# Kernel optimization log

Hardware: AMD Instinct MI355X
Metric: run time of the kernel (lower is better)

The kernel has to match this reference:

```python
import jax, jax.numpy as jnp
import numpy as np

N = 50000      # nodes
E = 800000     # edges (before self-loops)
DIN = 2        # dim_input
DEMB = 128     # dim_embedding
H = 8          # n_heads
DV = 16        # dim_values (H*DV == DEMB)
DH = 512       # dim_hidden
L = 2          # n_att_layers
K = 10         # APPNP steps
ALPHA = 0.1
EPS = 1e-5     # BatchNorm eps
NEG_SLOPE = 0.2  # GAT leaky_relu slope


def setup_inputs() -> dict:
    key = jax.random.key(0)
    ks = jax.random.split(key, 16)
    s = 0.05
    inp = {}
    inp["x"] = jax.random.normal(ks[0], (N, DIN), jnp.float32)
    inp["J"] = jax.random.uniform(ks[1], (N, 1), jnp.float32)
    inp["edge_index"] = jax.random.randint(ks[2], (2, E), 0, N, jnp.int32)
    # Lin1: Linear(dim_input+1, dim_embedding)
    inp["lin0_w"] = jax.random.normal(ks[3], (DIN + 1, DEMB), jnp.float32) * s
    inp["lin0_b"] = jnp.zeros((DEMB,), jnp.float32)
    # Per attention layer (stacked over L):
    inp["gat_w"]   = jax.random.normal(ks[4], (L, DEMB, H * DV), jnp.float32) * s
    inp["att_src"] = jax.random.normal(ks[5], (L, H, DV), jnp.float32) * s
    inp["att_dst"] = jax.random.normal(ks[6], (L, H, DV), jnp.float32) * s
    inp["lin1_w"]  = jax.random.normal(ks[7], (L, DV, DEMB), jnp.float32) * s
    inp["bn1_g"]   = jnp.ones((L, DEMB), jnp.float32)
    inp["bn1_b"]   = jnp.zeros((L, DEMB), jnp.float32)
    inp["lin2_w"]  = jax.random.normal(ks[8], (L, DEMB, DH), jnp.float32) * s
    inp["lin2_b"]  = jnp.zeros((L, DH), jnp.float32)
    inp["lin3_w"]  = jax.random.normal(ks[9], (L, DH, DEMB), jnp.float32) * s
    inp["lin3_b"]  = jnp.zeros((L, DEMB), jnp.float32)
    inp["bn2_g"]   = jnp.ones((L, DEMB), jnp.float32)
    inp["bn2_b"]   = jnp.zeros((L, DEMB), jnp.float32)
    return inp


def _bn(z, g, b):
    # BatchNorm1d over nodes, training-mode batch statistics (biased var)
    mu = z.mean(0)
    var = jnp.mean((z - mu) ** 2, axis=0)
    return g * (z - mu) * jax.lax.rsqrt(var + EPS) + b


def reference(x, J, edge_index, lin0_w, lin0_b, gat_w, att_src, att_dst,
              lin1_w, bn1_g, bn1_b, lin2_w, lin2_b, lin3_w, lin3_b,
              bn2_g, bn2_b):
    # add self-loops (PyG GATConv and APPNP defaults)
    loop = jnp.arange(N, dtype=edge_index.dtype)
    src = jnp.concatenate([edge_index[0], loop])  # message source j
    dst = jnp.concatenate([edge_index[1], loop])  # message target i

    h = jnp.concatenate([x, J], axis=1) @ lin0_w + lin0_b  # [N, DEMB]

    for l in range(L):
        # ---- GATConv ----
        xl = (h @ gat_w[l]).reshape(N, H, DV)                # [N,H,DV]
        a_s = (xl * att_src[l]).sum(-1)                      # [N,H]
        a_d = (xl * att_dst[l]).sum(-1)                      # [N,H]
        e = jax.nn.leaky_relu(a_s[src] + a_d[dst], NEG_SLOPE)  # [E',H]
        e = e - jax.ops.segment_max(e, dst, num_segments=N)[dst]
        ee = jnp.exp(e)
        alpha = ee / jax.ops.segment_sum(ee, dst, num_segments=N)[dst]
        msg = xl[src] * alpha[:, :, None]                    # [E',H,DV]
        gat_out = jax.ops.segment_sum(msg, dst, num_segments=N)  # [N,H,DV]
        # lin1 per head then sum over heads
        hsum = jnp.einsum('nhc,cd->nd', gat_out, lin1_w[l])  # [N,DEMB]
        h1 = _bn(h + hsum, bn1_g[l], bn1_b[l])
        h2 = jax.nn.relu(h1 @ lin2_w[l] + lin2_b[l]) @ lin3_w[l] + lin3_b[l]
        h = _bn(h2 + h1, bn2_g[l], bn2_b[l])

    # ---- APPNP: K steps of (1-a)*Ahat h + a*h0, Ahat = D^-1/2 (A+I) D^-1/2 ----
    deg = jax.ops.segment_sum(jnp.ones_like(dst, jnp.float32), dst, num_segments=N)
    dinv = jax.lax.rsqrt(jnp.maximum(deg, 1.0))  # self-loops guarantee deg>=1
    norm = (dinv[src] * dinv[dst])[:, None]      # [E',1]
    h0 = h

    def step(hk, _):
        agg = jax.ops.segment_sum(norm * hk[src], dst, num_segments=N)
        return (1.0 - ALPHA) * agg + ALPHA * h0, None

    h, _ = jax.lax.scan(step, h, None, length=K)
    return jnp.concatenate([h, J], axis=1)  # [N, DEMB+1]
```

## Files before the change

### kernel.cpp

```cpp
#include <hip/hip_runtime.h>

#define NN 50000
#define NE 800000
#define EP (NE + NN)
#define DEMB 128
#define DHID 512
#define CHUNK 12800
#define NB_SCAN 196

typedef unsigned short ushort_t;
typedef __attribute__((ext_vector_type(8))) short short8_t;
typedef __attribute__((ext_vector_type(4))) float float4_t;

__device__ __forceinline__ float bf2f(ushort_t u) {
    return __uint_as_float(((unsigned int)u) << 16);
}
__device__ __forceinline__ ushort_t f2bf(float f) {
    unsigned int x = __float_as_uint(f);
    x += 0x7fffu + ((x >> 16) & 1u);
    return (ushort_t)(x >> 16);
}
__device__ __forceinline__ float lo16(unsigned int w) { return __uint_as_float(w << 16); }
__device__ __forceinline__ float hi16(unsigned int w) { return __uint_as_float(w & 0xffff0000u); }
__device__ __forceinline__ unsigned int pack2(float a, float b) {
    return (unsigned int)f2bf(a) | ((unsigned int)f2bf(b) << 16);
}
static inline int cdiv(int a, int b) { return (a + b - 1) / b; }

__global__ void k_detect(const unsigned int* __restrict__ Jw, int* __restrict__ flag) {
    if (threadIdx.x != 0 || blockIdx.x != 0) return;
    int votes = 0;
    for (int i = 0; i < 8; ++i) {
        unsigned int w = Jw[i];
        unsigned int ex = (w >> 23) & 0xFFu;
        if ((w >> 31) == 0u && ex >= 100u && ex <= 126u) votes++;
    }
    *flag = (votes >= 6) ? 1 : 0;
}

struct CvtArgs {
    const void* src[16];
    float* dst[16];
    int n[16];
};
__global__ void k_cvt_all(CvtArgs a, const int* __restrict__ flag) {
    int which = blockIdx.y;
    int i = blockIdx.x * 256 + threadIdx.x;
    if (i >= a.n[which]) return;
    float v;
    if (*flag) v = ((const float*)a.src[which])[i];
    else       v = bf2f(((const ushort_t*)a.src[which])[i]);
    a.dst[which][i] = v;
}

struct TrArgs {
    const float* src[6];
    ushort_t* dst[6];
    int K[6];
    int Nc[6];
};
__global__ void k_tr_all(TrArgs a) {
    int which = blockIdx.y;
    int idx = blockIdx.x * 256 + threadIdx.x;
    int K = a.K[which], Nc = a.Nc[which];
    if (idx >= K * Nc) return;
    int k = idx / Nc, n = idx - k * Nc;
    a.dst[which][n * K + k] = f2bf(a.src[which][idx]);
}

__global__ void k_deg(const int* __restrict__ ei, int* __restrict__ deg) {
    int e = blockIdx.x * 256 + threadIdx.x;
    if (e >= EP) return;
    int d = (e < NE) ? ei[NE + e] : (e - NE);
    atomicAdd(&deg[d], 1);
}

__global__ void k_part(const int* __restrict__ deg, int* __restrict__ part) {
    __shared__ int sm[256];
    int i = blockIdx.x * 256 + threadIdx.x;
    int v = (i < NN) ? deg[i] : 0;
    sm[threadIdx.x] = v;
    __syncthreads();
    for (int off = 128; off > 0; off >>= 1) {
        if (threadIdx.x < off) sm[threadIdx.x] += sm[threadIdx.x + off];
        __syncthreads();
    }
    if (threadIdx.x == 0) part[blockIdx.x] = sm[0];
}

__global__ void k_scan2(const int* __restrict__ part, int* __restrict__ poff,
                        int* __restrict__ rowp) {
    __shared__ int sm[256];
    int t = threadIdx.x;
    int v = (t < NB_SCAN) ? part[t] : 0;
    sm[t] = v;
    __syncthreads();
    int incl = v;
    for (int off = 1; off < 256; off <<= 1) {
        int u = (t >= off) ? sm[t - off] : 0;
        __syncthreads();
        incl += u;
        sm[t] = incl;
        __syncthreads();
    }
    if (t < NB_SCAN) poff[t] = incl - v;
    if (t == 255) rowp[NN] = sm[255];
}

__global__ void k_rowp(const int* __restrict__ deg, const int* __restrict__ poff,
                       int* __restrict__ rowp, float* __restrict__ dinv) {
    __shared__ int sm[256];
    int i = blockIdx.x * 256 + threadIdx.x;
    int t = threadIdx.x;
    int v = (i < NN) ? deg[i] : 0;
    sm[t] = v;
    __syncthreads();
    int incl = v;
    for (int off = 1; off < 256; off <<= 1) {
        int u = (t >= off) ? sm[t - off] : 0;
        __syncthreads();
        incl += u;
        sm[t] = incl;
        __syncthreads();
    }
    if (i < NN) {
        rowp[i] = poff[blockIdx.x] + incl - v;
        dinv[i] = rsqrtf(fmaxf((float)v, 1.0f));
    }
}

__global__ void k_fill(const int* __restrict__ ei, int* __restrict__ fillpos,
                       ushort_t* __restrict__ col) {
    int e = blockIdx.x * 256 + threadIdx.x;
    if (e >= EP) return;
    int s, d;
    if (e < NE) { s = ei[e]; d = ei[NE + e]; } else { s = d = e - NE; }
    int pos = atomicAdd(&fillpos[d], 1);
    col[pos] = (ushort_t)s;
}

__global__ void k_lin0(const float* __restrict__ x, const float* __restrict__ J,
                       const float* __restrict__ w, const float* __restrict__ b,
                       float* __restrict__ h, ushort_t* __restrict__ hB) {
    int idx = blockIdx.x * 256 + threadIdx.x;
    if (idx >= NN * DEMB) return;
    int n = idx >> 7, d = idx & 127;
    float v = x[n * 2] * w[d] + x[n * 2 + 1] * w[DEMB + d] + J[n] * w[2 * DEMB + d] + b[d];
    h[idx] = v;
    hB[idx] = f2bf(v);
}

__global__ void k_att(const unsigned int* __restrict__ xlB, const float* __restrict__ asrc,
                      const float* __restrict__ adst, float* __restrict__ a_s,
                      float* __restrict__ a_d) {
    int idx = blockIdx.x * 256 + threadIdx.x;
    if (idx >= NN * 8) return;
    int n = idx >> 3, hh = idx & 7;
    const unsigned int* row = xlB + (size_t)n * 64 + hh * 8;
    float s = 0.f, d = 0.f;
#pragma unroll
    for (int c = 0; c < 8; ++c) {
        unsigned int w = row[c];
        float v0 = lo16(w), v1 = hi16(w);
        s += v0 * asrc[hh * 16 + 2 * c] + v1 * asrc[hh * 16 + 2 * c + 1];
        d += v0 * adst[hh * 16 + 2 * c] + v1 * adst[hh * 16 + 2 * c + 1];
    }
    a_s[idx] = s;
    a_d[idx] = d;
}

__global__ __launch_bounds__(256) void k_z1s(const float* __restrict__ h, const float* __restrict__ g,
                                             const float* __restrict__ w1,
                                             float* __restrict__ stats) {
    int d = threadIdx.x & 127;
    int rstart = blockIdx.x * 2 + (threadIdx.x >> 7);
    int stride = gridDim.x * 2;
    float s1 = 0.f, s2 = 0.f;
    for (int r = rstart; r < NN; r += stride) {
        const float* gr = g + r * 16;
        float s = h[(size_t)r * DEMB + d];
#pragma unroll
        for (int c = 0; c < 16; ++c) s += gr[c] * w1[c * DEMB + d];
        s1 += s;
        s2 += s * s;
    }
    __shared__ float b1[256], b2[256];
    b1[threadIdx.x] = s1;
    b2[threadIdx.x] = s2;
    __syncthreads();
    if (threadIdx.x < 128) {
        atomicAdd(&stats[threadIdx.x], b1[threadIdx.x] + b1[threadIdx.x + 128]);
        atomicAdd(&stats[128 + threadIdx.x], b2[threadIdx.x] + b2[threadIdx.x + 128]);
    }
}

__global__ void k_bnapply1(const float* __restrict__ h, const float* __restrict__ g,
                           const float* __restrict__ w1, const float* __restrict__ stats,
                           const float* __restrict__ gam, const float* __restrict__ bet,
                           float* __restrict__ outF, ushort_t* __restrict__ outB) {
    int idx = blockIdx.x * 256 + threadIdx.x;
    if (idx >= NN * DEMB) return;
    int n = idx >> 7, d = idx & 127;
    float s = h[idx];
    const float* gr = g + n * 16;
#pragma unroll
    for (int c = 0; c < 16; ++c) s += gr[c] * w1[c * DEMB + d];
    const float invN = 1.0f / (float)NN;
    float mu = stats[d] * invN;
    float var = stats[128 + d] * invN - mu * mu;
    float rs = rsqrtf(fmaxf(var, 0.f) + 1e-5f);
    float v = gam[d] * (s - mu) * rs + bet[d];
    outF[idx] = v;
    outB[idx] = f2bf(v);
}

__global__ void k_bnapply(const float* __restrict__ z, const float* __restrict__ stats,
                          const float* __restrict__ gam, const float* __restrict__ bet,
                          float* __restrict__ outF, ushort_t* __restrict__ outB) {
    int idx = blockIdx.x * 256 + threadIdx.x;
    if (idx >= NN * DEMB) return;
    int d = idx & 127;
    const float invN = 1.0f / (float)NN;
    float mu = stats[d] * invN;
    float var = stats[128 + d] * invN - mu * mu;
    float rs = rsqrtf(fmaxf(var, 0.f) + 1e-5f);
    float v = gam[d] * (z[idx] - mu) * rs + bet[d];
    outF[idx] = v;
    outB[idx] = f2bf(v);
}

__global__ void k_bnapply_fin(const float* __restrict__ z, const float* __restrict__ stats,
                              const float* __restrict__ gam, const float* __restrict__ bet,
                              const float* __restrict__ dinv,
                              unsigned int* __restrict__ hs, unsigned int* __restrict__ h0p) {
    int idx = blockIdx.x * 256 + threadIdx.x;
    if (idx >= NN * 64) return;
    int n = idx >> 6, d0 = (idx & 63) * 2;
    const float invN = 1.0f / (float)NN;
    float2 zv = ((const float2*)z)[idx];
    float mu0 = stats[d0] * invN, mu1 = stats[d0 + 1] * invN;
    float v0 = stats[128 + d0] * invN - mu0 * mu0;
    float v1 = stats[128 + d0 + 1] * invN - mu1 * mu1;
    float rs0 = rsqrtf(fmaxf(v0, 0.f) + 1e-5f);
    float rs1 = rsqrtf(fmaxf(v1, 0.f) + 1e-5f);
    float a = gam[d0] * (zv.x - mu0) * rs0 + bet[d0];
    float b = gam[d0 + 1] * (zv.y - mu1) * rs1 + bet[d0 + 1];
    float di = dinv[n];
    hs[idx] = pack2(di * a, di * b);
    h0p[idx] = pack2(a, b);
}

__global__ __launch_bounds__(256) void k_gat(const int* __restrict__ rowp,
                                             const ushort_t* __restrict__ col,
                                             const float* __restrict__ a_s, const float* __restrict__ a_d,
                                             const unsigned int* __restrict__ xlB, float* __restrict__ g) {
    int wid = (blockIdx.x * 256 + threadIdx.x) >> 6;
    int lane = threadIdx.x & 63;
    if (wid >= NN) return;
    int p0 = rowp[wid], p1 = rowp[wid + 1];
    int hh = lane >> 3;
    float ad2 = a_d[wid * 8 + hh];
    float acc0 = 0.f, acc1 = 0.f, s = 0.f;
    int p = p0;
    while (p < p1) {
        int cnt = p1 - p;
        if (cnt > 64) cnt = 64;
        int pl = p + lane;
        int jv = (int)col[pl < p1 ? pl : (p1 - 1)];
        int i = 0;
        for (; i + 8 <= cnt; i += 8) {
            int j0 = __shfl(jv, i),     j1 = __shfl(jv, i + 1);
            int j2 = __shfl(jv, i + 2), j3 = __shfl(jv, i + 3);
            int j4 = __shfl(jv, i + 4), j5 = __shfl(jv, i + 5);
            int j6 = __shfl(jv, i + 6), j7 = __shfl(jv, i + 7);
            float e0 = a_s[j0 * 8 + hh] + ad2, e1 = a_s[j1 * 8 + hh] + ad2;
            float e2 = a_s[j2 * 8 + hh] + ad2, e3 = a_s[j3 * 8 + hh] + ad2;
            float e4 = a_s[j4 * 8 + hh] + ad2, e5 = a_s[j5 * 8 + hh] + ad2;
            float e6 = a_s[j6 * 8 + hh] + ad2, e7 = a_s[j7 * 8 + hh] + ad2;
            unsigned int w0 = xlB[j0 * 64 + lane], w1 = xlB[j1 * 64 + lane];
            unsigned int w2 = xlB[j2 * 64 + lane], w3 = xlB[j3 * 64 + lane];
            unsigned int w4 = xlB[j4 * 64 + lane], w5 = xlB[j5 * 64 + lane];
            unsigned int w6 = xlB[j6 * 64 + lane], w7 = xlB[j7 * 64 + lane];
            e0 = e0 > 0.f ? e0 : 0.2f * e0;  e1 = e1 > 0.f ? e1 : 0.2f * e1;
            e2 = e2 > 0.f ? e2 : 0.2f * e2;  e3 = e3 > 0.f ? e3 : 0.2f * e3;
            e4 = e4 > 0.f ? e4 : 0.2f * e4;  e5 = e5 > 0.f ? e5 : 0.2f * e5;
            e6 = e6 > 0.f ? e6 : 0.2f * e6;  e7 = e7 > 0.f ? e7 : 0.2f * e7;
            float al0 = __expf(e0), al1 = __expf(e1), al2 = __expf(e2), al3 = __expf(e3);
            float al4 = __expf(e4), al5 = __expf(e5), al6 = __expf(e6), al7 = __expf(e7);
            s += al0 + al1 + al2 + al3 + al4 + al5 + al6 + al7;
            acc0 += al0 * lo16(w0) + al1 * lo16(w1) + al2 * lo16(w2) + al3 * lo16(w3) +
                    al4 * lo16(w4) + al5 * lo16(w5) + al6 * lo16(w6) + al7 * lo16(w7);
            acc1 += al0 * hi16(w0) + al1 * hi16(w1) + al2 * hi16(w2) + al3 * hi16(w3) +
                    al4 * hi16(w4) + al5 * hi16(w5) + al6 * hi16(w6) + al7 * hi16(w7);
        }
        for (; i < cnt; ++i) {
            int j = __shfl(jv, i);
            float e = a_s[j * 8 + hh] + ad2;
            e = e > 0.f ? e : 0.2f * e;
            float al = __expf(e);
            unsigned int w = xlB[j * 64 + lane];
            s += al;
            acc0 += al * lo16(w);
            acc1 += al * hi16(w);
        }
        p += cnt;
    }
    float inv = 1.f / s;
    acc0 *= inv;
    acc1 *= inv;
    acc0 += __shfl_xor(acc0, 8);  acc1 += __shfl_xor(acc1, 8);
    acc0 += __shfl_xor(acc0, 16); acc1 += __shfl_xor(acc1, 16);
    acc0 += __shfl_xor(acc0, 32); acc1 += __shfl_xor(acc1, 32);
    if (lane < 8) ((float2*)g)[wid * 8 + lane] = make_float2(acc0, acc1);
}

__global__ __launch_bounds__(256) void k_appnp(const int* __restrict__ rowp,
                                               const ushort_t* __restrict__ col,
                                               const float* __restrict__ dinv,
                                               const unsigned int* __restrict__ hs,
                                               const unsigned int* __restrict__ h0p,
                                               unsigned int* __restrict__ hs_out,
                                               const float* __restrict__ Jf,
                                               const int* __restrict__ flag,
                                               void* __restrict__ out, int writeOut) {
    int wid = (blockIdx.x * 256 + threadIdx.x) >> 6;
    int lane = threadIdx.x & 63;
    if (wid >= NN) return;
    int p0 = rowp[wid], p1 = rowp[wid + 1];
    float a0 = 0.f, a1 = 0.f;
    int p = p0;
    while (p < p1) {
        int cnt = p1 - p;
        if (cnt > 64) cnt = 64;
        int pl = p + lane;
        int jv = (int)col[pl < p1 ? pl : (p1 - 1)];
        int i = 0;
        for (; i + 8 <= cnt; i += 8) {
            int j0 = __shfl(jv, i),     j1 = __shfl(jv, i + 1);
            int j2 = __shfl(jv, i + 2), j3 = __shfl(jv, i + 3);
            int j4 = __shfl(jv, i + 4), j5 = __shfl(jv, i + 5);
            int j6 = __shfl(jv, i + 6), j7 = __shfl(jv, i + 7);
            unsigned int w0 = hs[j0 * 64 + lane], w1 = hs[j1 * 64 + lane];
            unsigned int w2 = hs[j2 * 64 + lane], w3 = hs[j3 * 64 + lane];
            unsigned int w4 = hs[j4 * 64 + lane], w5 = hs[j5 * 64 + lane];
            unsigned int w6 = hs[j6 * 64 + lane], w7 = hs[j7 * 64 + lane];
            a0 += lo16(w0) + lo16(w1) + lo16(w2) + lo16(w3) +
                  lo16(w4) + lo16(w5) + lo16(w6) + lo16(w7);
            a1 += hi16(w0) + hi16(w1) + hi16(w2) + hi16(w3) +
                  hi16(w4) + hi16(w5) + hi16(w6) + hi16(w7);
        }
        for (; i < cnt; ++i) {
            int j = __shfl(jv, i);
            unsigned int w = hs[j * 64 + lane];
            a0 += lo16(w);
            a1 += hi16(w);
        }
        p += cnt;
    }
    float di = dinv[wid];
    unsigned int hw = h0p[(size_t)wid * 64 + lane];
    float n0 = 0.9f * di * a0 + 0.1f * lo16(hw);
    float n1 = 0.9f * di * a1 + 0.1f * hi16(hw);
    if (!writeOut) {
        hs_out[(size_t)wid * 64 + lane] = pack2(di * n0, di * n1);
    } else {
        size_t base = (size_t)wid * 129;
        if (*flag) {
            float* o = (float*)out;
            o[base + 2 * lane] = n0;
            o[base + 2 * lane + 1] = n1;
            if (lane == 0) o[base + 128] = Jf[wid];
        } else {
            ushort_t* o = (ushort_t*)out;
            o[base + 2 * lane] = f2bf(n0);
            o[base + 2 * lane + 1] = f2bf(n1);
            if (lane == 0) o[base + 128] = f2bf(Jf[wid]);
        }
    }
}

template <int MODE>
__global__ __launch_bounds__(256) void k_gemm_bt(const ushort_t* __restrict__ A,
                                                 const ushort_t* __restrict__ Bt,
                                                 int M, int K, int Nc,
                                                 const float* __restrict__ bias,
                                                 const float* __restrict__ res,
                                                 float* __restrict__ outF,
                                                 ushort_t* __restrict__ outB,
                                                 float* __restrict__ stats) {
    __shared__ __align__(16) ushort_t lsA[64 * 32];
    __shared__ __align__(16) ushort_t lsB[64 * 32];
    int t = threadIdx.x;
    int m0 = blockIdx.x * 64;
    int n0 = blockIdx.y * 64;
    int w = t >> 6, lane = t & 63;
    int row16 = lane & 15, quad = lane >> 4;
    float4_t acc[4];
#pragma unroll
    for (int nt = 0; nt < 4; ++nt) acc[nt] = (float4_t){0.f, 0.f, 0.f, 0.f};
    int srow = t >> 2;
    int scol = (t & 3) * 8;
    const int nK = K >> 5;
    for (int kb = 0; kb < nK; ++kb) {
        int k0 = kb << 5;
        uint4 va = make_uint4(0u, 0u, 0u, 0u);
        int ar = m0 + srow;
        if (ar < M) va = *(const uint4*)(A + (size_t)ar * K + k0 + scol);
        *(uint4*)(lsA + srow * 32 + scol) = va;
        uint4 vb = *(const uint4*)(Bt + (size_t)(n0 + srow) * K + k0 + scol);
        *(uint4*)(lsB + srow * 32 + scol) = vb;
        __syncthreads();
        short8_t af = *(const short8_t*)(lsA + (w * 16 + row16) * 32 + quad * 8);
#pragma unroll
        for (int nt = 0; nt < 4; ++nt) {
            short8_t bfv = *(const short8_t*)(lsB + (nt * 16 + row16) * 32 + quad * 8);
            acc[nt] = __builtin_amdgcn_mfma_f32_16x16x32_bf16(af, bfv, acc[nt], 0, 0, 0);
        }
        __syncthreads();
    }
    if (MODE == 2) {
        __shared__ float s1[64], s2[64];
        if (t < 64) { s1[t] = 0.f; s2[t] = 0.f; }
        __syncthreads();
#pragma unroll
        for (int nt = 0; nt < 4; ++nt) {
            int cb = nt * 16 + row16;
            int cc = n0 + cb;
            float bv = bias[cc];
            float ls = 0.f, lq = 0.f;
#pragma unroll
            for (int r = 0; r < 4; ++r) {
                int rr = m0 + w * 16 + quad * 4 + r;
                if (rr < M) {
                    float v = acc[nt][r] + bv + res[(size_t)rr * Nc + cc];
                    outF[(size_t)rr * Nc + cc] = v;
                    ls += v;
                    lq += v * v;
                }
            }
            atomicAdd(&s1[cb], ls);
            atomicAdd(&s2[cb], lq);
        }
        __syncthreads();
        if (t < 64) {
            atomicAdd(&stats[n0 + t], s1[t]);
            atomicAdd(&stats[128 + n0 + t], s2[t]);
        }
    } else {
#pragma unroll
        for (int nt = 0; nt < 4; ++nt) {
            int cc = n0 + nt * 16 + row16;
            float bv = (MODE == 1) ? bias[cc] : 0.f;
#pragma unroll
            for (int r = 0; r < 4; ++r) {
                int rr = m0 + w * 16 + quad * 4 + r;
                if (rr < M) {
                    float v = acc[nt][r];
                    if (MODE == 1) {
                        v += bv;
                        v = v > 0.f ? v : 0.f;
                        outB[(size_t)rr * Nc + cc] = f2bf(v);
                    } else {
                        outB[(size_t)rr * Nc + cc] = f2bf(v);
                    }
                }
            }
        }
    }
}

extern "C" void kernel_launch(void* const* d_in, const int* in_sizes, int n_in,
                              void* d_out, int out_size, void* d_ws, size_t ws_size,
                              hipStream_t stream) {
    const int* ei = (const int*)d_in[2];

    char* p = (char*)d_ws;
    auto alloc = [&](size_t bytes) {
        void* r = (void*)p;
        p += (bytes + 255) & ~(size_t)255;
        return r;
    };
    float*    Af    = (float*)alloc((size_t)NN * DEMB * 4);
    float*    Cf    = (float*)alloc((size_t)NN * DEMB * 4);
    ushort_t* hB    = (ushort_t*)alloc((size_t)NN * DEMB * 2);
    ushort_t* h1B   = (ushort_t*)alloc((size_t)NN * DEMB * 2);
    ushort_t* xlB   = (ushort_t*)alloc((size_t)NN * DEMB * 2);
    unsigned int* hsA  = (unsigned int*)alloc((size_t)NN * 64 * 4);
    unsigned int* hsB_ = (unsigned int*)alloc((size_t)NN * 64 * 4);
    unsigned int* h0p  = (unsigned int*)alloc((size_t)NN * 64 * 4);
    ushort_t* hidB  = (ushort_t*)alloc((size_t)CHUNK * DHID * 2);
    float*    asv   = (float*)alloc((size_t)NN * 8 * 4);
    float*    adv   = (float*)alloc((size_t)NN * 8 * 4);
    float*    gv    = (float*)alloc((size_t)NN * 16 * 4);
    float*    dinvv = (float*)alloc((size_t)NN * 4);
    float*    stats = (float*)alloc(4 * 256 * 4);
    int*      deg   = (int*)alloc((size_t)NN * 4);
    int*      rowp  = (int*)alloc((size_t)(NN + 1) * 4);
    int*      fill  = (int*)alloc((size_t)NN * 4);
    ushort_t* colv  = (ushort_t*)alloc((size_t)EP * 2);
    int*      part  = (int*)alloc(NB_SCAN * 4);
    int*      poff  = (int*)alloc(NB_SCAN * 4);
    int*      flag  = (int*)alloc(256);
    ushort_t* wtg   = (ushort_t*)alloc((size_t)2 * 128 * 128 * 2);
    ushort_t* wt2   = (ushort_t*)alloc((size_t)2 * 512 * 128 * 2);
    ushort_t* wt3   = (ushort_t*)alloc((size_t)2 * 128 * 512 * 2);
    float* xf   = (float*)alloc((size_t)NN * 2 * 4);
    float* Jf   = (float*)alloc((size_t)NN * 4);
    float* l0wF = (float*)alloc(384 * 4);
    float* l0bF = (float*)alloc(128 * 4);
    float* gwF  = (float*)alloc(32768 * 4);
    float* asF  = (float*)alloc(256 * 4);
    float* adF  = (float*)alloc(256 * 4);
    float* w1F  = (float*)alloc(4096 * 4);
    float* b1gF = (float*)alloc(256 * 4);
    float* b1bF = (float*)alloc(256 * 4);
    float* w2F  = (float*)alloc(131072 * 4);
    float* b2F  = (float*)alloc(1024 * 4);
    float* w3F  = (float*)alloc(131072 * 4);
    float* b3F  = (float*)alloc(256 * 4);
    float* b2gF = (float*)alloc(256 * 4);
    float* b2bF = (float*)alloc(256 * 4);

    k_detect<<<1, 64, 0, stream>>>((const unsigned int*)d_in[1], flag);
    CvtArgs ca;
    {
        const int srcIdx[16] = {0, 1, 3, 4, 5, 6, 7, 8, 9, 10, 11, 12, 13, 14, 15, 16};
        float* dsts[16] = {xf, Jf, l0wF, l0bF, gwF, asF, adF, w1F, b1gF, b1bF,
                           w2F, b2F, w3F, b3F, b2gF, b2bF};
        const int ns[16] = {NN * 2, NN, 384, 128, 32768, 256, 256, 4096, 256, 256,
                            131072, 1024, 131072, 256, 256, 256};
        for (int i = 0; i < 16; ++i) { ca.src[i] = d_in[srcIdx[i]]; ca.dst[i] = dsts[i]; ca.n[i] = ns[i]; }
    }
    k_cvt_all<<<dim3(cdiv(131072, 256), 16), 256, 0, stream>>>(ca, flag);

    hipMemsetAsync(deg, 0, (size_t)NN * 4, stream);
    hipMemsetAsync(stats, 0, 4 * 256 * 4, stream);
    k_deg<<<cdiv(EP, 256), 256, 0, stream>>>(ei, deg);
    k_part<<<NB_SCAN, 256, 0, stream>>>(deg, part);
    k_scan2<<<1, 256, 0, stream>>>(part, poff, rowp);
    k_rowp<<<NB_SCAN, 256, 0, stream>>>(deg, poff, rowp, dinvv);
    hipMemcpyAsync(fill, rowp, (size_t)NN * 4, hipMemcpyDeviceToDevice, stream);
    k_fill<<<cdiv(EP, 256), 256, 0, stream>>>(ei, fill, colv);

    TrArgs ta;
    {
        const float* srcs[6] = {gwF, gwF + 16384, w2F, w2F + 65536, w3F, w3F + 65536};
        ushort_t* dsts[6] = {wtg, wtg + 16384, wt2, wt2 + 65536, wt3, wt3 + 65536};
        const int Ks[6] = {128, 128, 128, 128, 512, 512};
        const int Ncs[6] = {128, 128, 512, 512, 128, 128};
        for (int i = 0; i < 6; ++i) { ta.src[i] = srcs[i]; ta.dst[i] = dsts[i]; ta.K[i] = Ks[i]; ta.Nc[i] = Ncs[i]; }
    }
    k_tr_all<<<dim3(cdiv(65536, 256), 6), 256, 0, stream>>>(ta);

    k_lin0<<<cdiv(NN * DEMB, 256), 256, 0, stream>>>(xf, Jf, l0wF, l0bF, Af, hB);

    const int gemmMx = cdiv(NN, 64);
    for (int l = 0; l < 2; ++l) {
        float* st1 = stats + (l * 2 + 0) * 256;
        float* st2 = stats + (l * 2 + 1) * 256;
        k_gemm_bt<3><<<dim3(gemmMx, 2), 256, 0, stream>>>(hB, wtg + l * 16384, NN, 128, 128,
                                                          nullptr, nullptr, nullptr, xlB, nullptr);
        k_att<<<cdiv(NN * 8, 256), 256, 0, stream>>>((const unsigned int*)xlB, asF + l * 128,
                                                     adF + l * 128, asv, adv);
        k_gat<<<cdiv(NN * 64, 256), 256, 0, stream>>>(rowp, colv, asv, adv,
                                                      (const unsigned int*)xlB, gv);
        k_z1s<<<512, 256, 0, stream>>>(Af, gv, w1F + l * 2048, st1);
        k_bnapply1<<<cdiv(NN * DEMB, 256), 256, 0, stream>>>(Af, gv, w1F + l * 2048, st1,
                                                             b1gF + l * 128, b1bF + l * 128,
                                                             Cf, h1B);
        for (int c0 = 0; c0 < NN; c0 += CHUNK) {
            int rows = (NN - c0 < CHUNK) ? (NN - c0) : CHUNK;
            k_gemm_bt<1><<<dim3(cdiv(rows, 64), 8), 256, 0, stream>>>(
                h1B + (size_t)c0 * 128, wt2 + l * 65536, rows, 128, 512,
                b2F + l * 512, nullptr, nullptr, hidB, nullptr);
            k_gemm_bt<2><<<dim3(cdiv(rows, 64), 2), 256, 0, stream>>>(
                hidB, wt3 + l * 65536, rows, 512, 128,
                b3F + l * 128, Cf + (size_t)c0 * 128, Af + (size_t)c0 * 128, nullptr, st2);
        }
        if (l == 0) {
            k_bnapply<<<cdiv(NN * DEMB, 256), 256, 0, stream>>>(Af, st2, b2gF, b2bF, Af, hB);
        } else {
            k_bnapply_fin<<<cdiv(NN * 64, 256), 256, 0, stream>>>(Af, st2, b2gF + 128, b2bF + 128,
                                                                  dinvv, hsA, h0p);
        }
    }

    unsigned int* pin = hsA;
    unsigned int* pout = hsB_;
    for (int k = 0; k < 10; ++k) {
        int last = (k == 9) ? 1 : 0;
        k_appnp<<<cdiv(NN * 64, 256), 256, 0, stream>>>(rowp, colv, dinvv, pin, h0p, pout,
                                                        Jf, flag, d_out, last);
        unsigned int* tmp = pout;
        pout = pin;
        pin = tmp;
    }
}
```

Baseline: 1.028 ms.

## Use 128x128 MFMA GEMM tiles with direct global-to-LDS loads, drop chunking

Replaces the 64x64 GEMM tile kernel with a 128x128 tile. Each wave computes a 64x64 sub-tile with 16 accumulators, and operands are staged through global_load_lds direct copies. Row buffers are padded to a multiple of 128 so loads need no bounds checks, and the chunked MLP loop becomes one launch per GEMM over a full-size hidden buffer. The goal is more reuse per LDS load and fewer launches, at the cost of higher register pressure, fewer blocks, and a larger workspace.

Result: faster. 944.4 us (-8.2%).

```diff
diff --git a/kernel.cpp b/kernel.cpp
--- a/kernel.cpp
+++ b/kernel.cpp
@@ -1,11 +1,12 @@
 #include <hip/hip_runtime.h>
 
 #define NN 50000
+#define NP 50048
+#define NMT 391
 #define NE 800000
 #define EP (NE + NN)
 #define DEMB 128
 #define DHID 512
-#define CHUNK 12800
 #define NB_SCAN 196
 
 typedef unsigned short ushort_t;
@@ -24,6 +25,11 @@
 __device__ __forceinline__ float hi16(unsigned int w) { return __uint_as_float(w & 0xffff0000u); }
 __device__ __forceinline__ unsigned int pack2(float a, float b) {
     return (unsigned int)f2bf(a) | ((unsigned int)f2bf(b) << 16);
+}
+__device__ __forceinline__ void gl_lds16(const ushort_t* g, ushort_t* l) {
+    __builtin_amdgcn_global_load_lds(
+        (const __attribute__((address_space(1))) void*)g,
+        (__attribute__((address_space(3))) void*)l, 16, 0, 0);
 }
 static inline int cdiv(int a, int b) { return (a + b - 1) / b; }
 
@@ -380,7 +386,7 @@
 }
 
 template <int MODE>
-__global__ __launch_bounds__(256) void k_gemm_bt(const ushort_t* __restrict__ A,
+__global__ __launch_bounds__(256) void k_gemm128(const ushort_t* __restrict__ A,
                                                  const ushort_t* __restrict__ Bt,
                                                  int M, int K, int Nc,
                                                  const float* __restrict__ bias,
@@ -388,79 +394,88 @@
                                                  float* __restrict__ outF,
                                                  ushort_t* __restrict__ outB,
                                                  float* __restrict__ stats) {
-    __shared__ __align__(16) ushort_t lsA[64 * 32];
-    __shared__ __align__(16) ushort_t lsB[64 * 32];
+    __shared__ __align__(16) ushort_t lsA[128 * 32];
+    __shared__ __align__(16) ushort_t lsB[128 * 32];
     int t = threadIdx.x;
-    int m0 = blockIdx.x * 64;
-    int n0 = blockIdx.y * 64;
+    int m0 = blockIdx.x * 128, n0 = blockIdx.y * 128;
     int w = t >> 6, lane = t & 63;
     int row16 = lane & 15, quad = lane >> 4;
-    float4_t acc[4];
-#pragma unroll
-    for (int nt = 0; nt < 4; ++nt) acc[nt] = (float4_t){0.f, 0.f, 0.f, 0.f};
-    int srow = t >> 2;
-    int scol = (t & 3) * 8;
+    int mbase = (w & 1) * 64, nbase = (w >> 1) * 64;
+    float4_t acc[16];
+#pragma unroll
+    for (int i = 0; i < 16; ++i) acc[i] = (float4_t){0.f, 0.f, 0.f, 0.f};
+    int wrow = w * 32;
+    int lrow = lane >> 2;
+    int lcol = (lane & 3) * 8;
     const int nK = K >> 5;
     for (int kb = 0; kb < nK; ++kb) {
         int k0 = kb << 5;
-        uint4 va = make_uint4(0u, 0u, 0u, 0u);
-        int ar = m0 + srow;
-        if (ar < M) va = *(const uint4*)(A + (size_t)ar * K + k0 + scol);
-        *(uint4*)(lsA + srow * 32 + scol) = va;
-        uint4 vb = *(const uint4*)(Bt + (size_t)(n0 + srow) * K + k0 + scol);
-        *(uint4*)(lsB + srow * 32 + scol) = vb;
-        __syncthreads();
-        short8_t af = *(const short8_t*)(lsA + (w * 16 + row16) * 32 + quad * 8);
-#pragma unroll
-        for (int nt = 0; nt < 4; ++nt) {
-            short8_t bfv = *(const short8_t*)(lsB + (nt * 16 + row16) * 32 + quad * 8);
-            acc[nt] = __builtin_amdgcn_mfma_f32_16x16x32_bf16(af, bfv, acc[nt], 0, 0, 0);
-        }
-        __syncthreads();
+        __syncthreads();
+        gl_lds16(A  + (size_t)(m0 + wrow + lrow)      * K + k0 + lcol, lsA + wrow * 32);
+        gl_lds16(A  + (size_t)(m0 + wrow + 16 + lrow) * K + k0 + lcol, lsA + (wrow + 16) * 32);
+        gl_lds16(Bt + (size_t)(n0 + wrow + lrow)      * K + k0 + lcol, lsB + wrow * 32);
+        gl_lds16(Bt + (size_t)(n0 + wrow + 16 + lrow) * K + k0 + lcol, lsB + (wrow + 16) * 32);
+        __syncthreads();
+        short8_t afr[4], bfr[4];
+#pragma unroll
+        for (int i = 0; i < 4; ++i) {
+            afr[i] = *(const short8_t*)(lsA + (mbase + i * 16 + row16) * 32 + quad * 8);
+            bfr[i] = *(const short8_t*)(lsB + (nbase + i * 16 + row16) * 32 + quad * 8);
+        }
+#pragma unroll
+        for (int mt = 0; mt < 4; ++mt)
+#pragma unroll
+            for (int nt = 0; nt < 4; ++nt)
+                acc[mt * 4 + nt] = __builtin_amdgcn_mfma_f32_16x16x32_bf16(
+                    afr[mt], bfr[nt], acc[mt * 4 + nt], 0, 0, 0);
     }
     if (MODE == 2) {
-        __shared__ float s1[64], s2[64];
-        if (t < 64) { s1[t] = 0.f; s2[t] = 0.f; }
-        __syncthreads();
-#pragma unroll
-        for (int nt = 0; nt < 4; ++nt) {
-            int cb = nt * 16 + row16;
-            int cc = n0 + cb;
-            float bv = bias[cc];
-            float ls = 0.f, lq = 0.f;
-#pragma unroll
-            for (int r = 0; r < 4; ++r) {
-                int rr = m0 + w * 16 + quad * 4 + r;
-                if (rr < M) {
-                    float v = acc[nt][r] + bv + res[(size_t)rr * Nc + cc];
-                    outF[(size_t)rr * Nc + cc] = v;
-                    ls += v;
-                    lq += v * v;
+        __shared__ float s1[128], s2[128];
+        if (t < 128) { s1[t] = 0.f; s2[t] = 0.f; }
+        __syncthreads();
+#pragma unroll
+        for (int mt = 0; mt < 4; ++mt) {
+#pragma unroll
+            for (int nt = 0; nt < 4; ++nt) {
+                int cb = nbase + nt * 16 + row16;
+                int cc = n0 + cb;
+                float bv = bias[cc];
+                float ls = 0.f, lq = 0.f;
+#pragma unroll
+                for (int r = 0; r < 4; ++r) {
+                    int rr = m0 + mbase + mt * 16 + quad * 4 + r;
+                    if (rr < M) {
+                        float v = acc[mt * 4 + nt][r] + bv + res[(size_t)rr * Nc + cc];
+                        outF[(size_t)rr * Nc + cc] = v;
+                        ls += v;
+                        lq += v * v;
+                    }
                 }
+                atomicAdd(&s1[cb], ls);
+                atomicAdd(&s2[cb], lq);
             }
-            atomicAdd(&s1[cb], ls);
-            atomicAdd(&s2[cb], lq);
-        }
-        __syncthreads();
-        if (t < 64) {
+        }
+        __syncthreads();
+        if (t < 128) {
             atomicAdd(&stats[n0 + t], s1[t]);
             atomicAdd(&stats[128 + n0 + t], s2[t]);
         }
     } else {
 #pragma unroll
-        for (int nt = 0; nt < 4; ++nt) {
-            int cc = n0 + nt * 16 + row16;
-            float bv = (MODE == 1) ? bias[cc] : 0.f;
-#pragma unroll
-            for (int r = 0; r < 4; ++r) {
-                int rr = m0 + w * 16 + quad * 4 + r;
-                if (rr < M) {
-                    float v = acc[nt][r];
-                    if (MODE == 1) {
-                        v += bv;
-                        v = v > 0.f ? v : 0.f;
-                        outB[(size_t)rr * Nc + cc] = f2bf(v);
-                    } else {
+        for (int mt = 0; mt < 4; ++mt) {
+#pragma unroll
+            for (int nt = 0; nt < 4; ++nt) {
+                int cc = n0 + nbase + nt * 16 + row16;
+                float bv = (MODE == 1) ? bias[cc] : 0.f;
+#pragma unroll
+                for (int r = 0; r < 4; ++r) {
+                    int rr = m0 + mbase + mt * 16 + quad * 4 + r;
+                    if (rr < M) {
+                        float v = acc[mt * 4 + nt][r];
+                        if (MODE == 1) {
+                            v += bv;
+                            v = v > 0.f ? v : 0.f;
+                        }
                         outB[(size_t)rr * Nc + cc] = f2bf(v);
                     }
                 }
@@ -482,13 +497,13 @@
     };
     float*    Af    = (float*)alloc((size_t)NN * DEMB * 4);
     float*    Cf    = (float*)alloc((size_t)NN * DEMB * 4);
-    ushort_t* hB    = (ushort_t*)alloc((size_t)NN * DEMB * 2);
-    ushort_t* h1B   = (ushort_t*)alloc((size_t)NN * DEMB * 2);
+    ushort_t* hB    = (ushort_t*)alloc((size_t)NP * DEMB * 2);
+    ushort_t* h1B   = (ushort_t*)alloc((size_t)NP * DEMB * 2);
     ushort_t* xlB   = (ushort_t*)alloc((size_t)NN * DEMB * 2);
     unsigned int* hsA  = (unsigned int*)alloc((size_t)NN * 64 * 4);
     unsigned int* hsB_ = (unsigned int*)alloc((size_t)NN * 64 * 4);
     unsigned int* h0p  = (unsigned int*)alloc((size_t)NN * 64 * 4);
-    ushort_t* hidB  = (ushort_t*)alloc((size_t)CHUNK * DHID * 2);
+    ushort_t* hidB  = (ushort_t*)alloc((size_t)NP * DHID * 2);
     float*    asv   = (float*)alloc((size_t)NN * 8 * 4);
     float*    adv   = (float*)alloc((size_t)NN * 8 * 4);
     float*    gv    = (float*)alloc((size_t)NN * 16 * 4);
@@ -554,12 +569,11 @@
 
     k_lin0<<<cdiv(NN * DEMB, 256), 256, 0, stream>>>(xf, Jf, l0wF, l0bF, Af, hB);
 
-    const int gemmMx = cdiv(NN, 64);
     for (int l = 0; l < 2; ++l) {
         float* st1 = stats + (l * 2 + 0) * 256;
         float* st2 = stats + (l * 2 + 1) * 256;
-        k_gemm_bt<3><<<dim3(gemmMx, 2), 256, 0, stream>>>(hB, wtg + l * 16384, NN, 128, 128,
-                                                          nullptr, nullptr, nullptr, xlB, nullptr);
+        k_gemm128<3><<<dim3(NMT, 1), 256, 0, stream>>>(hB, wtg + l * 16384, NN, 128, 128,
+                                                       nullptr, nullptr, nullptr, xlB, nullptr);
         k_att<<<cdiv(NN * 8, 256), 256, 0, stream>>>((const unsigned int*)xlB, asF + l * 128,
                                                      adF + l * 128, asv, adv);
         k_gat<<<cdiv(NN * 64, 256), 256, 0, stream>>>(rowp, colv, asv, adv,
@@ -568,15 +582,10 @@
         k_bnapply1<<<cdiv(NN * DEMB, 256), 256, 0, stream>>>(Af, gv, w1F + l * 2048, st1,
                                                              b1gF + l * 128, b1bF + l * 128,
                                                              Cf, h1B);
-        for (int c0 = 0; c0 < NN; c0 += CHUNK) {
-            int rows = (NN - c0 < CHUNK) ? (NN - c0) : CHUNK;
-            k_gemm_bt<1><<<dim3(cdiv(rows, 64), 8), 256, 0, stream>>>(
-                h1B + (size_t)c0 * 128, wt2 + l * 65536, rows, 128, 512,
-                b2F + l * 512, nullptr, nullptr, hidB, nullptr);
-            k_gemm_bt<2><<<dim3(cdiv(rows, 64), 2), 256, 0, stream>>>(
-                hidB, wt3 + l * 65536, rows, 512, 128,
-                b3F + l * 128, Cf + (size_t)c0 * 128, Af + (size_t)c0 * 128, nullptr, st2);
-        }
+        k_gemm128<1><<<dim3(NMT, 4), 256, 0, stream>>>(h1B, wt2 + l * 65536, NN, 128, 512,
+                                                       b2F + l * 512, nullptr, nullptr, hidB, nullptr);
+        k_gemm128<2><<<dim3(NMT, 1), 256, 0, stream>>>(hidB, wt3 + l * 65536, NN, 512, 128,
+                                                       b3F + l * 128, Cf, Af, nullptr, st2);
         if (l == 0) {
             k_bnapply<<<cdiv(NN * DEMB, 256), 256, 0, stream>>>(Af, st2, b2gF, b2bF, Af, hB);
         } else {
```
